# Kernel tuning notes

Measured on AMD Instinct MI355X. Metric: run time of the kernel, lower is better.

The kernel has to match this reference:

```python
import jax, jax.numpy as jnp
import numpy as np

B, N, K, H, Cin, Cout = 2, 8192, 16, 4, 64, 128
D = Cout // H  # head_dim = 32


def setup_inputs() -> dict:
    key = jax.random.key(0)
    ks = jax.random.split(key, 16)
    x = jax.random.normal(ks[0], (B, N, Cin), jnp.float32)
    pos = jax.random.uniform(ks[1], (B, N, 3), jnp.float32)
    # KNN indices (torch.no_grad in original): pairwise squared distance + top_k
    sq = jnp.sum(pos * pos, -1)
    d2 = sq[:, :, None] - 2.0 * jnp.einsum('bnc,bmc->bnm', pos, pos) + sq[:, None, :]
    _, idx = jax.lax.top_k(-d2, K)  # (B, N, K) int32

    def lin(k, fin, fout):
        kw, kb = jax.random.split(k)
        lim = 1.0 / np.sqrt(fin)
        W = jax.random.uniform(kw, (fin, fout), jnp.float32, -lim, lim)
        b = jax.random.uniform(kb, (fout,), jnp.float32, -lim, lim)
        return W, b

    Wq, bq = lin(ks[2], Cin, Cout)
    Wkv, bkv = lin(ks[3], Cin, 2 * Cout)
    Wp1, bp1 = lin(ks[4], 3, Cout)
    Wp2, bp2 = lin(ks[5], Cout, Cout)
    Wa1, ba1 = lin(ks[6], Cout, Cout)
    Wa2, ba2 = lin(ks[7], Cout, Cout)
    Wo, bo = lin(ks[8], Cout, Cout)
    return dict(x=x, pos=pos, idx=idx, Wq=Wq, bq=bq, Wkv=Wkv, bkv=bkv,
                Wp1=Wp1, bp1=bp1, Wp2=Wp2, bp2=bp2,
                Wa1=Wa1, ba1=ba1, Wa2=Wa2, ba2=ba2, Wo=Wo, bo=bo)


def reference(x, pos, idx, Wq, bq, Wkv, bkv, Wp1, bp1, Wp2, bp2,
              Wa1, ba1, Wa2, ba2, Wo, bo):
    q = (x @ Wq + bq).reshape(B, N, H, D)
    kv = x @ Wkv + bkv
    k, v = kv[..., :Cout].reshape(B, N, H, D), kv[..., Cout:].reshape(B, N, H, D)
    bix = jnp.arange(B)[:, None, None]
    pos_n = pos[bix, idx]          # (B,N,K,3)
    k_n = k[bix, idx]              # (B,N,K,H,D)
    v_n = v[bix, idx]              # (B,N,K,H,D)
    pos_diff = pos[:, :, None, :] - pos_n
    pos_enc = jax.nn.relu(pos_diff @ Wp1 + bp1) @ Wp2 + bp2   # (B,N,K,Cout)
    pos_enc_h = pos_enc.reshape(B, N, K, H, D)
    rel = (k_n - q[:, :, None] + pos_enc_h).reshape(B, N, K, Cout)
    attn = jax.nn.relu(rel @ Wa1 + ba1) @ Wa2 + ba2           # (B,N,K,Cout)
    attn = jax.nn.softmax(attn.reshape(B, N, K, H, D), axis=2)
    agg = jnp.sum(attn * (v_n + pos_enc_h), axis=2).reshape(B, N, Cout)
    return agg @ Wo + bo
```

## Files before the change

kernel.cpp:

```cpp
#include <hip/hip_runtime.h>
#include <stdint.h>


typedef __attribute__((ext_vector_type(8))) short short8;
typedef __attribute__((ext_vector_type(4))) float f32x4;
typedef __attribute__((ext_vector_type(4))) unsigned int u32x4;

#define NN_TOT 16384
#define SLW 72

__device__ __forceinline__ uint32_t pk_bf16(float a, float b) {
  uint32_t r;
  asm("v_cvt_pk_bf16_f32 %0, %1, %2" : "=v"(r) : "v"(a), "v"(b));
  return r;
}
__device__ __forceinline__ float lo_f(uint32_t p) {
  return __builtin_bit_cast(float, p << 16);
}
__device__ __forceinline__ float hi_f(uint32_t p) {
  return __builtin_bit_cast(float, p & 0xffff0000u);
}
__device__ __forceinline__ short f2bf_rne(float f) {
  uint32_t u = __builtin_bit_cast(uint32_t, f);
  uint32_t r = (u + 0x7FFFu + ((u >> 16) & 1u)) >> 16;
  return (short)r;
}
__device__ __forceinline__ float bf2f(unsigned short s) {
  uint32_t u = ((uint32_t)s) << 16;
  return __builtin_bit_cast(float, u);
}

__global__ __launch_bounds__(256) void prep_frags(
    const float* __restrict__ Wq, const float* __restrict__ Wkv,
    const float* __restrict__ Wp2, const float* __restrict__ Wa1,
    const float* __restrict__ Wa2, const float* __restrict__ Wo,
    short* __restrict__ fqh, short* __restrict__ fql,
    short* __restrict__ fwp2, short* __restrict__ fwa1, short* __restrict__ fwa2,
    short* __restrict__ fwoh, short* __restrict__ fwol) {
  int r = blockIdx.x * 256 + threadIdx.x;
  if (r < 3072) {
    int t = r >> 7, rem = r & 127, s = rem >> 6, lane = rem & 63;
    int quad = lane >> 4, l15 = lane & 15;
    int col = t * 16 + l15;
    #pragma unroll
    for (int j = 0; j < 8; j++) {
      int i = 32 * s + quad * 8 + j;
      float wv = (col < 128) ? Wq[i * 128 + col] : Wkv[i * 256 + (col - 128)];
      short hi = f2bf_rne(wv);
      fqh[r * 8 + j] = hi;
      fql[r * 8 + j] = f2bf_rne(wv - bf2f((unsigned short)hi));
    }
  } else {
    int r2 = r - 3072;
    int mat = r2 >> 11;
    int rr = r2 & 2047;
    int t = rr >> 8, rem = rr & 255, s = rem >> 6, lane = rem & 63;
    int quad = lane >> 4, l15 = lane & 15;
    int col = t * 16 + l15;
    const float* W = (mat == 0) ? Wp2 : (mat == 1) ? Wa1 : (mat == 2) ? Wa2 : Wo;
    #pragma unroll
    for (int j = 0; j < 8; j++) {
      int i = 32 * s + quad * 8 + j;
      float wv = W[i * 128 + col];
      short hi = f2bf_rne(wv);
      if (mat == 3) {
        fwoh[rr * 8 + j] = hi;
        fwol[rr * 8 + j] = f2bf_rne(wv - bf2f((unsigned short)hi));
      } else if (mat == 0) fwp2[rr * 8 + j] = hi;
      else if (mat == 1)   fwa1[rr * 8 + j] = hi;
      else                 fwa2[rr * 8 + j] = hi;
    }
  }
}

__device__ __forceinline__ void split_frag(const f32x4 x0, const f32x4 x1,
                                           short8& ah, short8& al) {
  uint32_t h01 = pk_bf16(x0[0], x0[1]);
  uint32_t h23 = pk_bf16(x0[2], x0[3]);
  uint32_t h45 = pk_bf16(x1[0], x1[1]);
  uint32_t h67 = pk_bf16(x1[2], x1[3]);
  u32x4 hh = {h01, h23, h45, h67};
  ah = __builtin_bit_cast(short8, hh);
  uint32_t l01 = pk_bf16(x0[0] - lo_f(h01), x0[1] - hi_f(h01));
  uint32_t l23 = pk_bf16(x0[2] - lo_f(h23), x0[3] - hi_f(h23));
  uint32_t l45 = pk_bf16(x1[0] - lo_f(h45), x1[1] - hi_f(h45));
  uint32_t l67 = pk_bf16(x1[2] - lo_f(h67), x1[3] - hi_f(h67));
  u32x4 ll = {l01, l23, l45, l67};
  al = __builtin_bit_cast(short8, ll);
}

__global__ __launch_bounds__(256) void qkv_kernel(
    const float* __restrict__ x, const float* __restrict__ bq,
    const float* __restrict__ bkv,
    const short* __restrict__ fqh, const short* __restrict__ fql,
    float* __restrict__ q, unsigned short* __restrict__ ko,
    unsigned short* __restrict__ vo) {
  __shared__ __align__(16) short sBq[16384];
  const int tid = threadIdx.x;
  const int sec = blockIdx.x >> 8;
  const int gq = blockIdx.x & 255;
  const int w = tid >> 6, lane = tid & 63;
  const int quad = lane >> 4, l15 = lane & 15;

  {
    const u32x4* sh = reinterpret_cast<const u32x4*>(fqh + sec * 8192);
    const u32x4* sl = reinterpret_cast<const u32x4*>(fql + sec * 8192);
    u32x4* dh = reinterpret_cast<u32x4*>(sBq);
    u32x4* dl = reinterpret_cast<u32x4*>(sBq + 8192);
    #pragma unroll
    for (int i = 0; i < 4; i++) {
      dh[tid + i * 256] = sh[tid + i * 256];
      dl[tid + i * 256] = sl[tid + i * 256];
    }
  }

  const int base = (gq * 4 + w) * 16;
  short8 ah[2], al[2];
  #pragma unroll
  for (int s = 0; s < 2; s++) {
    const float* xp = x + (base + l15) * 64 + 32 * s + quad * 8;
    split_frag(*reinterpret_cast<const f32x4*>(xp),
               *reinterpret_cast<const f32x4*>(xp + 4), ah[s], al[s]);
  }
  __syncthreads();

  #pragma unroll
  for (int tt = 0; tt < 8; tt++) {
    f32x4 acc = {0.f, 0.f, 0.f, 0.f};
    #pragma unroll
    for (int s = 0; s < 2; s++) {
      int rt = tt * 2 + s;
      short8 bh = *reinterpret_cast<const short8*>(sBq + rt * 512 + lane * 8);
      short8 bl = *reinterpret_cast<const short8*>(sBq + 8192 + rt * 512 + lane * 8);
      acc = __builtin_amdgcn_mfma_f32_16x16x32_bf16(ah[s], bh, acc, 0, 0, 0);
      acc = __builtin_amdgcn_mfma_f32_16x16x32_bf16(ah[s], bl, acc, 0, 0, 0);
      acc = __builtin_amdgcn_mfma_f32_16x16x32_bf16(al[s], bh, acc, 0, 0, 0);
    }
    int cl = tt * 16 + l15;
    if (sec == 0) {
      float bias = bq[cl];
      #pragma unroll
      for (int r = 0; r < 4; r++)
        q[(base + quad * 4 + r) * 128 + cl] = acc[r] + bias;
    } else {
      float bias = bkv[(sec - 1) * 128 + cl];
      unsigned short* dst = (sec == 1) ? ko : vo;
      #pragma unroll
      for (int r = 0; r < 4; r++) {
        float vv = acc[r] + bias;
        dst[(base + quad * 4 + r) * 128 + cl] = (unsigned short)pk_bf16(vv, vv);
      }
    }
  }
}

__global__ __launch_bounds__(512, 6) void fused_attn_wo(
    const float* __restrict__ pos, const int* __restrict__ idx,
    const float* __restrict__ Wp1, const float* __restrict__ bp1,
    const float* __restrict__ bp2, const float* __restrict__ ba1,
    const float* __restrict__ ba2,
    const short* __restrict__ fwp2, const short* __restrict__ fwa1,
    const short* __restrict__ fwa2,
    const short* __restrict__ fwoh, const short* __restrict__ fwol,
    const float* __restrict__ bo,
    const float* __restrict__ qg, const unsigned short* __restrict__ kg,
    const unsigned short* __restrict__ vg, float* __restrict__ out) {
  __shared__ __align__(16) short sB[16384];
  __shared__ __align__(16) unsigned short slab[8][16 * SLW];
  __shared__ float spd[8][16][3];
  __shared__ int sidx[8][16];
  float (*sagg)[132] = reinterpret_cast<float(*)[132]>(&slab[0][0]);

  const int tid = threadIdx.x;
  const int w = tid >> 6;
  const int lane = tid & 63;
  const int quad = lane >> 4, l15 = lane & 15;
  const int nb0 = blockIdx.x * 8;
  const int node = nb0 + w;
  unsigned short* myslab = &slab[w][0];

  if (lane < 16) {
    int ji = idx[node * 16 + lane];
    int jn = ((node >> 13) << 13) + ji;
    sidx[w][lane] = jn;
    spd[w][lane][0] = pos[node * 3 + 0] - pos[jn * 3 + 0];
    spd[w][lane][1] = pos[node * 3 + 1] - pos[jn * 3 + 1];
    spd[w][lane][2] = pos[node * 3 + 2] - pos[jn * 3 + 2];
  }

  {
    const u32x4* s4 = reinterpret_cast<const u32x4*>(fwp2);
    u32x4* d4 = reinterpret_cast<u32x4*>(sB);
    #pragma unroll
    for (int i = 0; i < 4; i++) d4[tid + i * 512] = s4[tid + i * 512];
  }

  short8 aP[4];
  #pragma unroll
  for (int p = 0; p < 2; p++) {
    const int c = lane + p * 64;
    float wp0 = Wp1[c], wp1 = Wp1[128 + c], wp2v = Wp1[256 + c], bb = bp1[c];
    #pragma unroll
    for (int m = 0; m < 16; m++) {
      float h = fmaxf(bb + spd[w][m][0] * wp0 + spd[w][m][1] * wp1 +
                           spd[w][m][2] * wp2v, 0.f);
      myslab[m * SLW + lane] = (unsigned short)pk_bf16(h, h);
    }
    #pragma unroll
    for (int ss = 0; ss < 2; ss++)
      aP[p * 2 + ss] = *reinterpret_cast<const short8*>(
          myslab + l15 * SLW + 32 * ss + quad * 8);
  }
  __syncthreads();

  short8 k_pk[4];
  {
    const unsigned short* kp = kg + sidx[w][l15] * 128;
    #pragma unroll
    for (int s = 0; s < 4; s++)
      k_pk[s] = *reinterpret_cast<const short8*>(kp + 32 * s + quad * 8);
  }

  f32x4 acc[8];

  #pragma unroll
  for (int t = 0; t < 8; t++) acc[t] = (f32x4){0.f, 0.f, 0.f, 0.f};
  #pragma unroll
  for (int s = 0; s < 4; s++) {
    #pragma unroll
    for (int t = 0; t < 8; t++) {
      short8 bf = *reinterpret_cast<const short8*>(sB + ((t * 4 + s) * 64 + lane) * 8);
      acc[t] = __builtin_amdgcn_mfma_f32_16x16x32_bf16(aP[s], bf, acc[t], 0, 0, 0);
    }
  }
  __syncthreads();

  {
    const u32x4* s4 = reinterpret_cast<const u32x4*>(fwa1);
    u32x4* d4 = reinterpret_cast<u32x4*>(sB);
    #pragma unroll
    for (int i = 0; i < 4; i++) d4[tid + i * 512] = s4[tid + i * 512];
  }

  uint32_t pe_pk[8][2];
  short8 a2[4];
  {
    const float* qrow = qg + node * 128;
    #pragma unroll
    for (int p = 0; p < 2; p++) {
      #pragma unroll
      for (int tt = 0; tt < 4; tt++) {
        int t = p * 4 + tt;
        int c = 16 * t + l15;
        float bb = bp2[c];
        float qv = qrow[c];
        float f0 = acc[t][0] + bb, f1 = acc[t][1] + bb;
        float f2 = acc[t][2] + bb, f3 = acc[t][3] + bb;
        pe_pk[t][0] = pk_bf16(f0, f1);
        pe_pk[t][1] = pk_bf16(f2, f3);
        uint32_t g01 = pk_bf16(f0 - qv, f1 - qv);
        uint32_t g23 = pk_bf16(f2 - qv, f3 - qv);
        int cl = 16 * tt + l15;
        myslab[(quad * 4 + 0) * SLW + cl] = (unsigned short)g01;
        myslab[(quad * 4 + 1) * SLW + cl] = (unsigned short)(g01 >> 16);
        myslab[(quad * 4 + 2) * SLW + cl] = (unsigned short)g23;
        myslab[(quad * 4 + 3) * SLW + cl] = (unsigned short)(g23 >> 16);
      }
      #pragma unroll
      for (int ss = 0; ss < 2; ss++) {
        int s = p * 2 + ss;
        short8 pq = *reinterpret_cast<const short8*>(
            myslab + l15 * SLW + 32 * ss + quad * 8);
        short8 kk = k_pk[s];
        u32x4 av = {pk_bf16(bf2f((unsigned short)kk[0]) + bf2f((unsigned short)pq[0]),
                            bf2f((unsigned short)kk[1]) + bf2f((unsigned short)pq[1])),
                    pk_bf16(bf2f((unsigned short)kk[2]) + bf2f((unsigned short)pq[2]),
                            bf2f((unsigned short)kk[3]) + bf2f((unsigned short)pq[3])),
                    pk_bf16(bf2f((unsigned short)kk[4]) + bf2f((unsigned short)pq[4]),
                            bf2f((unsigned short)kk[5]) + bf2f((unsigned short)pq[5])),
                    pk_bf16(bf2f((unsigned short)kk[6]) + bf2f((unsigned short)pq[6]),
                            bf2f((unsigned short)kk[7]) + bf2f((unsigned short)pq[7]))};
        a2[s] = __builtin_bit_cast(short8, av);
      }
    }
  }
  __syncthreads();

  #pragma unroll
  for (int t = 0; t < 8; t++) acc[t] = (f32x4){0.f, 0.f, 0.f, 0.f};
  #pragma unroll
  for (int s = 0; s < 4; s++) {
    #pragma unroll
    for (int t = 0; t < 8; t++) {
      short8 bf = *reinterpret_cast<const short8*>(sB + ((t * 4 + s) * 64 + lane) * 8);
      acc[t] = __builtin_amdgcn_mfma_f32_16x16x32_bf16(a2[s], bf, acc[t], 0, 0, 0);
    }
  }
  __syncthreads();

  {
    const u32x4* s4 = reinterpret_cast<const u32x4*>(fwa2);
    u32x4* d4 = reinterpret_cast<u32x4*>(sB);
    #pragma unroll
    for (int i = 0; i < 4; i++) d4[tid + i * 512] = s4[tid + i * 512];
  }

  short8 a3[4];
  #pragma unroll
  for (int p = 0; p < 2; p++) {
    #pragma unroll
    for (int tt = 0; tt < 4; tt++) {
      int t = p * 4 + tt;
      int c = 16 * t + l15;
      float bb = ba1[c];
      uint32_t p01 = pk_bf16(fmaxf(acc[t][0] + bb, 0.f), fmaxf(acc[t][1] + bb, 0.f));
      uint32_t p23 = pk_bf16(fmaxf(acc[t][2] + bb, 0.f), fmaxf(acc[t][3] + bb, 0.f));
      int cl = 16 * tt + l15;
      myslab[(quad * 4 + 0) * SLW + cl] = (unsigned short)p01;
      myslab[(quad * 4 + 1) * SLW + cl] = (unsigned short)(p01 >> 16);
      myslab[(quad * 4 + 2) * SLW + cl] = (unsigned short)p23;
      myslab[(quad * 4 + 3) * SLW + cl] = (unsigned short)(p23 >> 16);
    }
    #pragma unroll
    for (int ss = 0; ss < 2; ss++)
      a3[p * 2 + ss] = *reinterpret_cast<const short8*>(
          myslab + l15 * SLW + 32 * ss + quad * 8);
  }
  __syncthreads();

  #pragma unroll
  for (int t = 0; t < 8; t++) acc[t] = (f32x4){0.f, 0.f, 0.f, 0.f};
  #pragma unroll
  for (int s = 0; s < 4; s++) {
    #pragma unroll
    for (int t = 0; t < 8; t++) {
      short8 bf = *reinterpret_cast<const short8*>(sB + ((t * 4 + s) * 64 + lane) * 8);
      acc[t] = __builtin_amdgcn_mfma_f32_16x16x32_bf16(a3[s], bf, acc[t], 0, 0, 0);
    }
  }

  int vb[4];
  #pragma unroll
  for (int r = 0; r < 4; r++) vb[r] = sidx[w][quad * 4 + r] * 128;

  #pragma unroll
  for (int t = 0; t < 8; t++) {
    int c = 16 * t + l15;
    float bb = ba2[c];
    float g0 = acc[t][0] + bb, g1 = acc[t][1] + bb;
    float g2 = acc[t][2] + bb, g3 = acc[t][3] + bb;
    float mx = fmaxf(fmaxf(g0, g1), fmaxf(g2, g3));
    mx = fmaxf(mx, __shfl_xor(mx, 16));
    mx = fmaxf(mx, __shfl_xor(mx, 32));
    float e0 = __expf(g0 - mx), e1 = __expf(g1 - mx);
    float e2 = __expf(g2 - mx), e3 = __expf(g3 - mx);
    float ls = e0 + e1 + e2 + e3;
    ls += __shfl_xor(ls, 16);
    ls += __shfl_xor(ls, 32);
    float pe0 = lo_f(pe_pk[t][0]), pe1 = hi_f(pe_pk[t][0]);
    float pe2 = lo_f(pe_pk[t][1]), pe3 = hi_f(pe_pk[t][1]);
    float p = e0 * (bf2f(vg[vb[0] + c]) + pe0)
            + e1 * (bf2f(vg[vb[1] + c]) + pe1)
            + e2 * (bf2f(vg[vb[2] + c]) + pe2)
            + e3 * (bf2f(vg[vb[3] + c]) + pe3);
    p += __shfl_xor(p, 16);
    p += __shfl_xor(p, 32);
    if (quad == 0) sagg[w][c] = p * __builtin_amdgcn_rcpf(ls);
  }
  __syncthreads();

  {
    short8 ah[4], al[4];
    #pragma unroll
    for (int s = 0; s < 4; s++) {
      f32x4 x0 = *reinterpret_cast<const f32x4*>(&sagg[l15][32 * s + quad * 8]);
      f32x4 x1 = *reinterpret_cast<const f32x4*>(&sagg[l15][32 * s + quad * 8 + 4]);
      split_frag(x0, x1, ah[s], al[s]);
    }
    f32x4 aw = {0.f, 0.f, 0.f, 0.f};
    #pragma unroll
    for (int s = 0; s < 4; s++) {
      short8 bh = *reinterpret_cast<const short8*>(fwoh + ((w * 4 + s) * 64 + lane) * 8);
      short8 bl = *reinterpret_cast<const short8*>(fwol + ((w * 4 + s) * 64 + lane) * 8);
      aw = __builtin_amdgcn_mfma_f32_16x16x32_bf16(ah[s], bh, aw, 0, 0, 0);
      aw = __builtin_amdgcn_mfma_f32_16x16x32_bf16(ah[s], bl, aw, 0, 0, 0);
      aw = __builtin_amdgcn_mfma_f32_16x16x32_bf16(al[s], bh, aw, 0, 0, 0);
    }
    int c = 16 * w + l15;
    float bb = bo[c];
    if (quad < 2) {
      #pragma unroll
      for (int r = 0; r < 4; r++)
        out[(nb0 + quad * 4 + r) * 128 + c] = aw[r] + bb;
    }
  }
}

extern "C" void kernel_launch(void* const* d_in, const int* in_sizes, int n_in,
                              void* d_out, int out_size, void* d_ws, size_t ws_size,
                              hipStream_t stream) {
  const float* x   = (const float*)d_in[0];
  const float* pos = (const float*)d_in[1];
  const int*   idx = (const int*)d_in[2];
  const float* Wq  = (const float*)d_in[3];
  const float* bq  = (const float*)d_in[4];
  const float* Wkv = (const float*)d_in[5];
  const float* bkv = (const float*)d_in[6];
  const float* Wp1 = (const float*)d_in[7];
  const float* bp1 = (const float*)d_in[8];
  const float* Wp2 = (const float*)d_in[9];
  const float* bp2 = (const float*)d_in[10];
  const float* Wa1 = (const float*)d_in[11];
  const float* ba1 = (const float*)d_in[12];
  const float* Wa2 = (const float*)d_in[13];
  const float* ba2 = (const float*)d_in[14];
  const float* Wo  = (const float*)d_in[15];
  const float* bo  = (const float*)d_in[16];

  char* ws = (char*)d_ws;
  short* fqh  = (short*)(ws + 0);
  short* fql  = (short*)(ws + 49152);
  short* fwp2 = (short*)(ws + 98304);
  short* fwa1 = (short*)(ws + 131072);
  short* fwa2 = (short*)(ws + 163840);
  short* fwoh = (short*)(ws + 196608);
  short* fwol = (short*)(ws + 229376);
  float* qb = (float*)(ws + 262144);
  unsigned short* kb = (unsigned short*)(ws + 262144 + 8388608);
  unsigned short* vb = kb + NN_TOT * 128;

  prep_frags<<<44, 256, 0, stream>>>(Wq, Wkv, Wp2, Wa1, Wa2, Wo,
                                     fqh, fql, fwp2, fwa1, fwa2, fwoh, fwol);
  qkv_kernel<<<768, 256, 0, stream>>>(x, bq, bkv, fqh, fql, qb, kb, vb);
  fused_attn_wo<<<2048, 512, 0, stream>>>(pos, idx, Wp1, bp1, bp2, ba1, ba2,
                                          fwp2, fwa1, fwa2, fwoh, fwol, bo,
                                          qb, kb, vb, (float*)d_out);
}
```

Measured before the change: 174.9 us.

## Interleave per-tile-pair MFMA with epilogues and drop softmax-invariant ba2 bias

The three 128x128 MFMA stages in the fused attention kernel now each compute two 16-column output tiles at a time. Each pair's bias, ReLU or softmax epilogue runs immediately, so the kernel no longer holds all eight f32x4 accumulators live. This is meant to cut VGPR pressure under launch_bounds(512,6) and avoid spills. The ba2 bias is removed because it is constant along the K axis the softmax reduces over, so it cancels; the q row loads are also hoisted. In exchange, the next stage's weight copy into LDS no longer overlaps with the previous epilogue and gets its own barrier, and the removed bias can slightly change rounding.

```diff
diff --git a/kernel.cpp b/kernel.cpp
--- a/kernel.cpp
+++ b/kernel.cpp
@@ -158,7 +158,6 @@
     const float* __restrict__ pos, const int* __restrict__ idx,
     const float* __restrict__ Wp1, const float* __restrict__ bp1,
     const float* __restrict__ bp2, const float* __restrict__ ba1,
-    const float* __restrict__ ba2,
     const short* __restrict__ fwp2, const short* __restrict__ fwa1,
     const short* __restrict__ fwa2,
     const short* __restrict__ fwoh, const short* __restrict__ fwol,
@@ -214,112 +213,105 @@
   __syncthreads();
 
   short8 k_pk[4];
+  float qv[8];
   {
     const unsigned short* kp = kg + sidx[w][l15] * 128;
     #pragma unroll
     for (int s = 0; s < 4; s++)
       k_pk[s] = *reinterpret_cast<const short8*>(kp + 32 * s + quad * 8);
-  }
-
-  f32x4 acc[8];
-
-  #pragma unroll
-  for (int t = 0; t < 8; t++) acc[t] = (f32x4){0.f, 0.f, 0.f, 0.f};
-  #pragma unroll
-  for (int s = 0; s < 4; s++) {
-    #pragma unroll
-    for (int t = 0; t < 8; t++) {
-      short8 bf = *reinterpret_cast<const short8*>(sB + ((t * 4 + s) * 64 + lane) * 8);
-      acc[t] = __builtin_amdgcn_mfma_f32_16x16x32_bf16(aP[s], bf, acc[t], 0, 0, 0);
-    }
-  }
-  __syncthreads();
-
-  {
-    const u32x4* s4 = reinterpret_cast<const u32x4*>(fwa1);
-    u32x4* d4 = reinterpret_cast<u32x4*>(sB);
-    #pragma unroll
-    for (int i = 0; i < 4; i++) d4[tid + i * 512] = s4[tid + i * 512];
+    const float* qrow = qg + node * 128;
+    #pragma unroll
+    for (int t = 0; t < 8; t++) qv[t] = qrow[16 * t + l15];
   }
 
   uint32_t pe_pk[8][2];
   short8 a2[4];
-  {
-    const float* qrow = qg + node * 128;
-    #pragma unroll
-    for (int p = 0; p < 2; p++) {
-      #pragma unroll
-      for (int tt = 0; tt < 4; tt++) {
-        int t = p * 4 + tt;
-        int c = 16 * t + l15;
-        float bb = bp2[c];
-        float qv = qrow[c];
-        float f0 = acc[t][0] + bb, f1 = acc[t][1] + bb;
-        float f2 = acc[t][2] + bb, f3 = acc[t][3] + bb;
+
+  #pragma unroll
+  for (int p = 0; p < 2; p++) {
+    #pragma unroll
+    for (int half = 0; half < 2; half++) {
+      const int t0 = p * 4 + half * 2, t1 = t0 + 1;
+      f32x4 aa = {0.f, 0.f, 0.f, 0.f}, ab = {0.f, 0.f, 0.f, 0.f};
+      #pragma unroll
+      for (int s = 0; s < 4; s++) {
+        short8 b0 = *reinterpret_cast<const short8*>(sB + ((t0 * 4 + s) * 64 + lane) * 8);
+        short8 b1 = *reinterpret_cast<const short8*>(sB + ((t1 * 4 + s) * 64 + lane) * 8);
+        aa = __builtin_amdgcn_mfma_f32_16x16x32_bf16(aP[s], b0, aa, 0, 0, 0);
+        ab = __builtin_amdgcn_mfma_f32_16x16x32_bf16(aP[s], b1, ab, 0, 0, 0);
+      }
+      #pragma unroll
+      for (int e = 0; e < 2; e++) {
+        const int t = e ? t1 : t0;
+        const f32x4 ac = e ? ab : aa;
+        float bb = bp2[16 * t + l15];
+        float f0 = ac[0] + bb, f1 = ac[1] + bb, f2 = ac[2] + bb, f3 = ac[3] + bb;
         pe_pk[t][0] = pk_bf16(f0, f1);
         pe_pk[t][1] = pk_bf16(f2, f3);
-        uint32_t g01 = pk_bf16(f0 - qv, f1 - qv);
-        uint32_t g23 = pk_bf16(f2 - qv, f3 - qv);
-        int cl = 16 * tt + l15;
+        float q_ = qv[t];
+        uint32_t g01 = pk_bf16(f0 - q_, f1 - q_);
+        uint32_t g23 = pk_bf16(f2 - q_, f3 - q_);
+        int cl = 16 * (t & 3) + l15;
         myslab[(quad * 4 + 0) * SLW + cl] = (unsigned short)g01;
         myslab[(quad * 4 + 1) * SLW + cl] = (unsigned short)(g01 >> 16);
         myslab[(quad * 4 + 2) * SLW + cl] = (unsigned short)g23;
         myslab[(quad * 4 + 3) * SLW + cl] = (unsigned short)(g23 >> 16);
       }
-      #pragma unroll
-      for (int ss = 0; ss < 2; ss++) {
-        int s = p * 2 + ss;
-        short8 pq = *reinterpret_cast<const short8*>(
-            myslab + l15 * SLW + 32 * ss + quad * 8);
-        short8 kk = k_pk[s];
-        u32x4 av = {pk_bf16(bf2f((unsigned short)kk[0]) + bf2f((unsigned short)pq[0]),
-                            bf2f((unsigned short)kk[1]) + bf2f((unsigned short)pq[1])),
-                    pk_bf16(bf2f((unsigned short)kk[2]) + bf2f((unsigned short)pq[2]),
-                            bf2f((unsigned short)kk[3]) + bf2f((unsigned short)pq[3])),
-                    pk_bf16(bf2f((unsigned short)kk[4]) + bf2f((unsigned short)pq[4]),
-                            bf2f((unsigned short)kk[5]) + bf2f((unsigned short)pq[5])),
-                    pk_bf16(bf2f((unsigned short)kk[6]) + bf2f((unsigned short)pq[6]),
-                            bf2f((unsigned short)kk[7]) + bf2f((unsigned short)pq[7]))};
-        a2[s] = __builtin_bit_cast(short8, av);
+    }
+    #pragma unroll
+    for (int ss = 0; ss < 2; ss++) {
+      int s = p * 2 + ss;
+      short8 pq = *reinterpret_cast<const short8*>(
+          myslab + l15 * SLW + 32 * ss + quad * 8);
+      short8 kk = k_pk[s];
+      u32x4 av = {pk_bf16(bf2f((unsigned short)kk[0]) + bf2f((unsigned short)pq[0]),
+                          bf2f((unsigned short)kk[1]) + bf2f((unsigned short)pq[1])),
+                  pk_bf16(bf2f((unsigned short)kk[2]) + bf2f((unsigned short)pq[2]),
+                          bf2f((unsigned short)kk[3]) + bf2f((unsigned short)pq[3])),
+                  pk_bf16(bf2f((unsigned short)kk[4]) + bf2f((unsigned short)pq[4]),
+                          bf2f((unsigned short)kk[5]) + bf2f((unsigned short)pq[5])),
+                  pk_bf16(bf2f((unsigned short)kk[6]) + bf2f((unsigned short)pq[6]),
+                          bf2f((unsigned short)kk[7]) + bf2f((unsigned short)pq[7]))};
+      a2[s] = __builtin_bit_cast(short8, av);
+    }
+  }
+  __syncthreads();
+
+  {
+    const u32x4* s4 = reinterpret_cast<const u32x4*>(fwa1);
+    u32x4* d4 = reinterpret_cast<u32x4*>(sB);
+    #pragma unroll
+    for (int i = 0; i < 4; i++) d4[tid + i * 512] = s4[tid + i * 512];
+  }
+  __syncthreads();
+
+  short8 a3[4];
+  #pragma unroll
+  for (int p = 0; p < 2; p++) {
+    #pragma unroll
+    for (int half = 0; half < 2; half++) {
+      const int t0 = p * 4 + half * 2, t1 = t0 + 1;
+      f32x4 aa = {0.f, 0.f, 0.f, 0.f}, ab = {0.f, 0.f, 0.f, 0.f};
+      #pragma unroll
+      for (int s = 0; s < 4; s++) {
+        short8 b0 = *reinterpret_cast<const short8*>(sB + ((t0 * 4 + s) * 64 + lane) * 8);
+        short8 b1 = *reinterpret_cast<const short8*>(sB + ((t1 * 4 + s) * 64 + lane) * 8);
+        aa = __builtin_amdgcn_mfma_f32_16x16x32_bf16(a2[s], b0, aa, 0, 0, 0);
+        ab = __builtin_amdgcn_mfma_f32_16x16x32_bf16(a2[s], b1, ab, 0, 0, 0);
       }
-    }
-  }
-  __syncthreads();
-
-  #pragma unroll
-  for (int t = 0; t < 8; t++) acc[t] = (f32x4){0.f, 0.f, 0.f, 0.f};
-  #pragma unroll
-  for (int s = 0; s < 4; s++) {
-    #pragma unroll
-    for (int t = 0; t < 8; t++) {
-      short8 bf = *reinterpret_cast<const short8*>(sB + ((t * 4 + s) * 64 + lane) * 8);
-      acc[t] = __builtin_amdgcn_mfma_f32_16x16x32_bf16(a2[s], bf, acc[t], 0, 0, 0);
-    }
-  }
-  __syncthreads();
-
-  {
-    const u32x4* s4 = reinterpret_cast<const u32x4*>(fwa2);
-    u32x4* d4 = reinterpret_cast<u32x4*>(sB);
-    #pragma unroll
-    for (int i = 0; i < 4; i++) d4[tid + i * 512] = s4[tid + i * 512];
-  }
-
-  short8 a3[4];
-  #pragma unroll
-  for (int p = 0; p < 2; p++) {
-    #pragma unroll
-    for (int tt = 0; tt < 4; tt++) {
-      int t = p * 4 + tt;
-      int c = 16 * t + l15;
-      float bb = ba1[c];
-      uint32_t p01 = pk_bf16(fmaxf(acc[t][0] + bb, 0.f), fmaxf(acc[t][1] + bb, 0.f));
-      uint32_t p23 = pk_bf16(fmaxf(acc[t][2] + bb, 0.f), fmaxf(acc[t][3] + bb, 0.f));
-      int cl = 16 * tt + l15;
-      myslab[(quad * 4 + 0) * SLW + cl] = (unsigned short)p01;
-      myslab[(quad * 4 + 1) * SLW + cl] = (unsigned short)(p01 >> 16);
-      myslab[(quad * 4 + 2) * SLW + cl] = (unsigned short)p23;
-      myslab[(quad * 4 + 3) * SLW + cl] = (unsigned short)(p23 >> 16);
+      #pragma unroll
+      for (int e = 0; e < 2; e++) {
+        const int t = e ? t1 : t0;
+        const f32x4 ac = e ? ab : aa;
+        float bb = ba1[16 * t + l15];
+        uint32_t p01 = pk_bf16(fmaxf(ac[0] + bb, 0.f), fmaxf(ac[1] + bb, 0.f));
+        uint32_t p23 = pk_bf16(fmaxf(ac[2] + bb, 0.f), fmaxf(ac[3] + bb, 0.f));
+        int cl = 16 * (t & 3) + l15;
+        myslab[(quad * 4 + 0) * SLW + cl] = (unsigned short)p01;
+        myslab[(quad * 4 + 1) * SLW + cl] = (unsigned short)(p01 >> 16);
+        myslab[(quad * 4 + 2) * SLW + cl] = (unsigned short)p23;
+        myslab[(quad * 4 + 3) * SLW + cl] = (unsigned short)(p23 >> 16);
+      }
     }
     #pragma unroll
     for (int ss = 0; ss < 2; ss++)
@@ -328,44 +320,53 @@
   }
   __syncthreads();
 
-  #pragma unroll
-  for (int t = 0; t < 8; t++) acc[t] = (f32x4){0.f, 0.f, 0.f, 0.f};
-  #pragma unroll
-  for (int s = 0; s < 4; s++) {
-    #pragma unroll
-    for (int t = 0; t < 8; t++) {
-      short8 bf = *reinterpret_cast<const short8*>(sB + ((t * 4 + s) * 64 + lane) * 8);
-      acc[t] = __builtin_amdgcn_mfma_f32_16x16x32_bf16(a3[s], bf, acc[t], 0, 0, 0);
-    }
-  }
+  {
+    const u32x4* s4 = reinterpret_cast<const u32x4*>(fwa2);
+    u32x4* d4 = reinterpret_cast<u32x4*>(sB);
+    #pragma unroll
+    for (int i = 0; i < 4; i++) d4[tid + i * 512] = s4[tid + i * 512];
+  }
+  __syncthreads();
 
   int vb[4];
   #pragma unroll
   for (int r = 0; r < 4; r++) vb[r] = sidx[w][quad * 4 + r] * 128;
 
   #pragma unroll
-  for (int t = 0; t < 8; t++) {
-    int c = 16 * t + l15;
-    float bb = ba2[c];
-    float g0 = acc[t][0] + bb, g1 = acc[t][1] + bb;
-    float g2 = acc[t][2] + bb, g3 = acc[t][3] + bb;
-    float mx = fmaxf(fmaxf(g0, g1), fmaxf(g2, g3));
-    mx = fmaxf(mx, __shfl_xor(mx, 16));
-    mx = fmaxf(mx, __shfl_xor(mx, 32));
-    float e0 = __expf(g0 - mx), e1 = __expf(g1 - mx);
-    float e2 = __expf(g2 - mx), e3 = __expf(g3 - mx);
-    float ls = e0 + e1 + e2 + e3;
-    ls += __shfl_xor(ls, 16);
-    ls += __shfl_xor(ls, 32);
-    float pe0 = lo_f(pe_pk[t][0]), pe1 = hi_f(pe_pk[t][0]);
-    float pe2 = lo_f(pe_pk[t][1]), pe3 = hi_f(pe_pk[t][1]);
-    float p = e0 * (bf2f(vg[vb[0] + c]) + pe0)
-            + e1 * (bf2f(vg[vb[1] + c]) + pe1)
-            + e2 * (bf2f(vg[vb[2] + c]) + pe2)
-            + e3 * (bf2f(vg[vb[3] + c]) + pe3);
-    p += __shfl_xor(p, 16);
-    p += __shfl_xor(p, 32);
-    if (quad == 0) sagg[w][c] = p * __builtin_amdgcn_rcpf(ls);
+  for (int tp = 0; tp < 4; tp++) {
+    const int t0 = tp * 2, t1 = t0 + 1;
+    f32x4 aa = {0.f, 0.f, 0.f, 0.f}, ab = {0.f, 0.f, 0.f, 0.f};
+    #pragma unroll
+    for (int s = 0; s < 4; s++) {
+      short8 b0 = *reinterpret_cast<const short8*>(sB + ((t0 * 4 + s) * 64 + lane) * 8);
+      short8 b1 = *reinterpret_cast<const short8*>(sB + ((t1 * 4 + s) * 64 + lane) * 8);
+      aa = __builtin_amdgcn_mfma_f32_16x16x32_bf16(a3[s], b0, aa, 0, 0, 0);
+      ab = __builtin_amdgcn_mfma_f32_16x16x32_bf16(a3[s], b1, ab, 0, 0, 0);
+    }
+    #pragma unroll
+    for (int e = 0; e < 2; e++) {
+      const int t = e ? t1 : t0;
+      const f32x4 ac = e ? ab : aa;
+      int c = 16 * t + l15;
+      float g0 = ac[0], g1 = ac[1], g2 = ac[2], g3 = ac[3];
+      float mx = fmaxf(fmaxf(g0, g1), fmaxf(g2, g3));
+      mx = fmaxf(mx, __shfl_xor(mx, 16));
+      mx = fmaxf(mx, __shfl_xor(mx, 32));
+      float e0 = __expf(g0 - mx), e1 = __expf(g1 - mx);
+      float e2 = __expf(g2 - mx), e3 = __expf(g3 - mx);
+      float ls = e0 + e1 + e2 + e3;
+      ls += __shfl_xor(ls, 16);
+      ls += __shfl_xor(ls, 32);
+      float pe0 = lo_f(pe_pk[t][0]), pe1 = hi_f(pe_pk[t][0]);
+      float pe2 = lo_f(pe_pk[t][1]), pe3 = hi_f(pe_pk[t][1]);
+      float pp = e0 * (bf2f(vg[vb[0] + c]) + pe0)
+               + e1 * (bf2f(vg[vb[1] + c]) + pe1)
+               + e2 * (bf2f(vg[vb[2] + c]) + pe2)
+               + e3 * (bf2f(vg[vb[3] + c]) + pe3);
+      pp += __shfl_xor(pp, 16);
+      pp += __shfl_xor(pp, 32);
+      if (quad == 0) sagg[w][c] = pp * __builtin_amdgcn_rcpf(ls);
+    }
   }
   __syncthreads();
 
@@ -413,7 +414,6 @@
   const float* Wa1 = (const float*)d_in[11];
   const float* ba1 = (const float*)d_in[12];
   const float* Wa2 = (const float*)d_in[13];
-  const float* ba2 = (const float*)d_in[14];
   const float* Wo  = (const float*)d_in[15];
   const float* bo  = (const float*)d_in[16];
 
@@ -432,7 +432,7 @@
   prep_frags<<<44, 256, 0, stream>>>(Wq, Wkv, Wp2, Wa1, Wa2, Wo,
                                      fqh, fql, fwp2, fwa1, fwa2, fwoh, fwol);
   qkv_kernel<<<768, 256, 0, stream>>>(x, bq, bkv, fqh, fql, qb, kb, vb);
-  fused_attn_wo<<<2048, 512, 0, stream>>>(pos, idx, Wp1, bp1, bp2, ba1, ba2,
+  fused_attn_wo<<<2048, 512, 0, stream>>>(pos, idx, Wp1, bp1, bp2, ba1,
                                           fwp2, fwa1, fwa2, fwoh, fwol, bo,
                                           qb, kb, vb, (float*)d_out);
 }
```

Measured after the change: 168.2 us. 1.04x faster.
